# Kernel optimization log

Hardware: AMD Instinct MI355X
Metric: run time of the kernel (lower is better)

The kernel has to match this reference:

```python
import jax, jax.numpy as jnp
import numpy as np

IN_DIM = 2048
OUT_DIM = 2048
BASIS_DIM = 64
BATCH = 4
SEQ = 4096
EPS = 1e-5


def _make_bbasis():
    k = np.arange(BASIS_DIM, dtype=np.float64)[:, None]  # (K,1)
    i = np.arange(OUT_DIM, dtype=np.float64)[None, :]    # (1,D)
    return jnp.asarray(np.cos(2.0 * np.pi * (k + 1.0) / (i + 2.0)), dtype=jnp.float32)


def setup_inputs() -> dict:
    key = jax.random.key(0)
    k1, k2, k3, k4 = jax.random.split(key, 4)
    x = jax.random.normal(k1, (BATCH, SEQ, IN_DIM), dtype=jnp.float32)
    # nn.init.uniform_(-0.1, 0.1) style scaling for weights
    W = jax.random.uniform(k2, (OUT_DIM, IN_DIM), dtype=jnp.float32, minval=-0.1, maxval=0.1)
    W_res = jax.random.uniform(k3, (OUT_DIM, IN_DIM), dtype=jnp.float32, minval=-0.1, maxval=0.1)
    Acoeff = jax.random.uniform(k4, (OUT_DIM, BASIS_DIM), dtype=jnp.float32, minval=-0.1, maxval=0.1)
    gamma = jnp.ones((OUT_DIM,), dtype=jnp.float32)
    beta = jnp.zeros((OUT_DIM,), dtype=jnp.float32)
    Bbasis = _make_bbasis()
    return {"x": x, "W": W, "W_res": W_res, "gamma": gamma, "beta": beta,
            "Acoeff": Acoeff, "Bbasis": Bbasis}


def reference(x, W, W_res, gamma, beta, Acoeff, Bbasis):
    # residual projection (use_residual == 'separate')
    residual = jnp.einsum('bsi,oi->bso', x, W_res)          # (B,S,D)
    transformed = jnp.einsum('bsi,oi->bso', x, W)           # (B,S,D)
    # LayerNorm over last dim
    mean = jnp.mean(transformed, axis=-1, keepdims=True)
    var = jnp.mean(jnp.square(transformed - mean), axis=-1, keepdims=True)
    normalized = (transformed - mean) * jax.lax.rsqrt(var + EPS) * gamma + beta
    # periodic basis gather
    seq_len = x.shape[1]
    j = jnp.arange(seq_len) % BASIS_DIM                      # (S,)
    B_vec = Bbasis[j]                                        # (S,D)
    A_vec = Acoeff[:, j].T                                   # (S,D)
    scalars = jnp.einsum('bsd,sd->bs', normalized, B_vec)    # (B,S)
    return scalars[:, :, None] * A_vec[None] + residual      # (B,S,D)
```

## Files before the change

### kernel.cpp

```cpp
#include <hip/hip_runtime.h>
#include <hip/hip_bf16.h>

#define KDIM   2048
#define DDIM   2048
#define MROWS  16384
#define BASIS  64
#define EPSLN  1e-5f
#define NKT    32

typedef __bf16 bf16x8 __attribute__((ext_vector_type(8)));
typedef float  f32x4  __attribute__((ext_vector_type(4)));
typedef unsigned short u16x8 __attribute__((ext_vector_type(8)));

static __device__ __forceinline__ unsigned short f2bf(float f) {
  union { float f; unsigned int u; } v; v.f = f;
  unsigned int r = v.u + 0x7FFFu + ((v.u >> 16) & 1u);
  return (unsigned short)(r >> 16);
}
static __device__ __forceinline__ float bf2f(unsigned short h) {
  union { unsigned int u; float f; } v; v.u = ((unsigned int)h) << 16;
  return v.f;
}

__global__ __launch_bounds__(256) void cast_f32_bf16(
    const float* __restrict__ in, unsigned short* __restrict__ out, int n4) {
  int i = blockIdx.x * blockDim.x + threadIdx.x;
  int stride = gridDim.x * blockDim.x;
  for (; i < n4; i += stride) {
    float4 v = ((const float4*)in)[i];
    ushort4 o;
    o.x = f2bf(v.x); o.y = f2bf(v.y); o.z = f2bf(v.z); o.w = f2bf(v.w);
    ((ushort4*)out)[i] = o;
  }
}

__global__ __launch_bounds__(256) void transpose_acoeff(
    const float* __restrict__ Ac, float* __restrict__ At) {
  int j = blockIdx.x;
  for (int d = threadIdx.x; d < DDIM; d += blockDim.x)
    At[j * DDIM + d] = Ac[d * BASIS + j];
}

__device__ __forceinline__ void gload16(const void* g, void* l) {
  __builtin_amdgcn_global_load_lds(
      (const __attribute__((address_space(1))) unsigned int*)(unsigned long long)g,
      (__attribute__((address_space(3))) unsigned int*)(unsigned int)(unsigned long long)l,
      16, 0, 0);
}

__device__ __forceinline__ void bar() {
  asm volatile("s_barrier" ::: "memory");
}

__global__ __launch_bounds__(512, 2) void gemm_dual(
    const unsigned short* __restrict__ Abf,
    const unsigned short* __restrict__ Bbf,
    unsigned short* __restrict__ Tout,
    float* __restrict__ Rout)
{
  __shared__ __align__(16) unsigned short As[2 * 256 * 64];
  __shared__ __align__(16) unsigned short Bs[2 * 256 * 64];

  const int tid  = threadIdx.x;
  const int lane = tid & 63;
  const int wave = tid >> 6;

  const int bid = blockIdx.x;
  const int wg  = (bid & 7) * 128 + (bid >> 3);
  const int bm  = wg >> 4;
  const int bn  = wg & 15;
  const int brow0 = bm * 256;
  const int bcol0 = bn * 256;

  const int srow  = tid >> 3;
  const int sslot = (tid & 7) ^ (srow & 7);
  const unsigned short* pA = Abf + (size_t)(brow0 + srow) * KDIM + sslot * 8;
  const unsigned short* pB = Bbf + (size_t)(bcol0 + srow) * KDIM + sslot * 8;
  const int ldst = wave * 512;

  const int wm   = wave >> 2;
  const int wn   = wave & 3;
  const int frow = lane & 15;
  const int kgrp = lane >> 4;
  const int swz  = frow & 7;

  f32x4 acc[8][4] = {};

#pragma unroll
  for (int c = 0; c < 4; ++c) {
    gload16(pA + (size_t)c * 64 * KDIM,      As + c * 4096 + ldst);
    gload16(pB + (size_t)c * 64 * KDIM,      Bs + c * 4096 + ldst);
  }
#pragma unroll
  for (int c = 0; c < 4; ++c) {
    gload16(pA + (size_t)c * 64 * KDIM + 64, As + 16384 + c * 4096 + ldst);
    gload16(pB + (size_t)c * 64 * KDIM + 64, Bs + 16384 + c * 4096 + ldst);
  }

  for (int kt = 0; kt < NKT; ++kt) {
    const unsigned short* As_b = As + (kt & 1) * 16384;
    const unsigned short* Bs_b = Bs + (kt & 1) * 16384;

    if (kt < NKT - 1) { asm volatile("s_waitcnt vmcnt(8)" ::: "memory"); }
    else              { asm volatile("s_waitcnt vmcnt(0)" ::: "memory"); }
    __builtin_amdgcn_sched_barrier(0);
    bar();

#pragma unroll
    for (int ko = 0; ko < 2; ++ko) {
      bf16x8 bv[4], af[4];
#pragma unroll
      for (int j = 0; j < 4; ++j) {
        const int row = wn * 64 + j * 16 + frow;
        bv[j] = *(const bf16x8*)(Bs_b + row * 64 + (((ko * 4 + kgrp) ^ swz) << 3));
      }
#pragma unroll
      for (int i = 0; i < 4; ++i) {
        const int row = wm * 128 + i * 16 + frow;
        af[i] = *(const bf16x8*)(As_b + row * 64 + (((ko * 4 + kgrp) ^ swz) << 3));
      }
      bar();
      __builtin_amdgcn_s_setprio(1);
#pragma unroll
      for (int i = 0; i < 4; ++i)
#pragma unroll
        for (int j = 0; j < 4; ++j)
          acc[i][j] = __builtin_amdgcn_mfma_f32_16x16x32_bf16(af[i], bv[j], acc[i][j], 0, 0, 0);
      __builtin_amdgcn_s_setprio(0);
      bar();
#pragma unroll
      for (int i = 0; i < 4; ++i) {
        const int row = wm * 128 + 64 + i * 16 + frow;
        af[i] = *(const bf16x8*)(As_b + row * 64 + (((ko * 4 + kgrp) ^ swz) << 3));
      }
      bar();
      __builtin_amdgcn_s_setprio(1);
#pragma unroll
      for (int i = 0; i < 4; ++i)
#pragma unroll
        for (int j = 0; j < 4; ++j)
          acc[4 + i][j] = __builtin_amdgcn_mfma_f32_16x16x32_bf16(af[i], bv[j], acc[4 + i][j], 0, 0, 0);
      __builtin_amdgcn_s_setprio(0);
      bar();
    }

    if (kt + 2 < NKT) {
      unsigned short* Ad = As + (kt & 1) * 16384;
      unsigned short* Bd = Bs + (kt & 1) * 16384;
      const int k64 = (kt + 2) * 64;
#pragma unroll
      for (int c = 0; c < 4; ++c) {
        gload16(pA + (size_t)c * 64 * KDIM + k64, Ad + c * 4096 + ldst);
        gload16(pB + (size_t)c * 64 * KDIM + k64, Bd + c * 4096 + ldst);
      }
    }
  }

  if (bn < 8) {
    unsigned short* Cb = Tout;
    const int c0 = bcol0;
#pragma unroll
    for (int i = 0; i < 8; ++i) {
      const int r0 = brow0 + wm * 128 + i * 16 + kgrp * 4;
#pragma unroll
      for (int j = 0; j < 4; ++j) {
        const int col = c0 + wn * 64 + j * 16 + frow;
#pragma unroll
        for (int r = 0; r < 4; ++r)
          Cb[(size_t)(r0 + r) * DDIM + col] = f2bf(acc[i][j][r]);
      }
    }
  } else {
    float* Cb = Rout;
    const int c0 = bcol0 - 2048;
#pragma unroll
    for (int i = 0; i < 8; ++i) {
      const int r0 = brow0 + wm * 128 + i * 16 + kgrp * 4;
#pragma unroll
      for (int j = 0; j < 4; ++j) {
        const int col = c0 + wn * 64 + j * 16 + frow;
#pragma unroll
        for (int r = 0; r < 4; ++r)
          Cb[(size_t)(r0 + r) * DDIM + col] = acc[i][j][r];
      }
    }
  }
}

__global__ __launch_bounds__(256) void epilogue(
    const unsigned short* __restrict__ T, const float* __restrict__ Bb,
    const float* __restrict__ At, const float* __restrict__ gam,
    const float* __restrict__ bet, float* __restrict__ out)
{
  __shared__ float red[16];
  const int row = blockIdx.x;
  const int s   = row & 4095;
  const int j   = s & 63;
  const int tid = threadIdx.x;
  const size_t rb = (size_t)row * DDIM;
  const int d0 = tid * 8;

  u16x8 tv = *(const u16x8*)(T + rb + d0);
  float t[8];
#pragma unroll
  for (int k = 0; k < 8; ++k) t[k] = bf2f(tv[k]);

  float sum = 0.f, sq = 0.f;
#pragma unroll
  for (int k = 0; k < 8; ++k) { sum += t[k]; sq += t[k] * t[k]; }
#pragma unroll
  for (int off = 32; off > 0; off >>= 1) {
    sum += __shfl_down(sum, off);
    sq  += __shfl_down(sq,  off);
  }
  if ((tid & 63) == 0) { red[tid >> 6] = sum; red[4 + (tid >> 6)] = sq; }
  __syncthreads();
  if (tid == 0) {
    float sAll = red[0] + red[1] + red[2] + red[3];
    float qAll = red[4] + red[5] + red[6] + red[7];
    float m = sAll * (1.0f / 2048.0f);
    float v = qAll * (1.0f / 2048.0f) - m * m;
    red[8] = m;
    red[9] = rsqrtf(v + EPSLN);
  }
  __syncthreads();
  const float mean = red[8], rstd = red[9];

  const size_t jb = (size_t)j * DDIM;
  float4 g0 = *(const float4*)(gam + d0), g1 = *(const float4*)(gam + d0 + 4);
  float4 b0 = *(const float4*)(bet + d0), b1 = *(const float4*)(bet + d0 + 4);
  float4 w0 = *(const float4*)(Bb + jb + d0), w1 = *(const float4*)(Bb + jb + d0 + 4);

  float sc =
      ((t[0] - mean) * rstd * g0.x + b0.x) * w0.x +
      ((t[1] - mean) * rstd * g0.y + b0.y) * w0.y +
      ((t[2] - mean) * rstd * g0.z + b0.z) * w0.z +
      ((t[3] - mean) * rstd * g0.w + b0.w) * w0.w +
      ((t[4] - mean) * rstd * g1.x + b1.x) * w1.x +
      ((t[5] - mean) * rstd * g1.y + b1.y) * w1.y +
      ((t[6] - mean) * rstd * g1.z + b1.z) * w1.z +
      ((t[7] - mean) * rstd * g1.w + b1.w) * w1.w;
#pragma unroll
  for (int off = 32; off > 0; off >>= 1) sc += __shfl_down(sc, off);
  if ((tid & 63) == 0) red[10 + (tid >> 6)] = sc;
  __syncthreads();
  const float scalar = red[10] + red[11] + red[12] + red[13];

  float4 a0 = *(const float4*)(At + jb + d0), a1 = *(const float4*)(At + jb + d0 + 4);
  float4 o0 = *(const float4*)(out + rb + d0), o1 = *(const float4*)(out + rb + d0 + 4);
  o0.x = scalar * a0.x + o0.x;  o0.y = scalar * a0.y + o0.y;
  o0.z = scalar * a0.z + o0.z;  o0.w = scalar * a0.w + o0.w;
  o1.x = scalar * a1.x + o1.x;  o1.y = scalar * a1.y + o1.y;
  o1.z = scalar * a1.z + o1.z;  o1.w = scalar * a1.w + o1.w;
  *(float4*)(out + rb + d0)     = o0;
  *(float4*)(out + rb + d0 + 4) = o1;
}

extern "C" void kernel_launch(void* const* d_in, const int* in_sizes, int n_in,
                              void* d_out, int out_size, void* d_ws, size_t ws_size,
                              hipStream_t stream) {
  const float* x      = (const float*)d_in[0];
  const float* W      = (const float*)d_in[1];
  const float* Wres   = (const float*)d_in[2];
  const float* gamma  = (const float*)d_in[3];
  const float* beta   = (const float*)d_in[4];
  const float* Acoeff = (const float*)d_in[5];
  const float* Bbasis = (const float*)d_in[6];
  float* out = (float*)d_out;
  char* ws = (char*)d_ws;

  unsigned short* xbf = (unsigned short*)ws;
  unsigned short* Wc  = (unsigned short*)(ws + 67108864);
  unsigned short* T   = (unsigned short*)(ws + 83886080);
  float* At           = (float*)(ws + 150994944);

  cast_f32_bf16<<<2048, 256, 0, stream>>>(x,    xbf,            8388608);
  cast_f32_bf16<<<512,  256, 0, stream>>>(W,    Wc,             1048576);
  cast_f32_bf16<<<512,  256, 0, stream>>>(Wres, Wc + 4194304,   1048576);
  transpose_acoeff<<<64, 256, 0, stream>>>(Acoeff, At);

  gemm_dual<<<1024, 512, 0, stream>>>(xbf, Wc, T, out);

  epilogue<<<16384, 256, 0, stream>>>(T, Bbasis, At, gamma, beta, out);
}
```

Baseline: 612.2 us.

## Fuse prep kernels, interleave GEMM prefetch with MFMA phases, store residual as bf16

Merges the three cast launches and the Acoeff transpose into one prep kernel. Restructures the GEMM main loop into four MFMA phases, spreading the next-tile global-to-LDS loads across them instead of issuing them all at the end of each k-step. The residual half of the GEMM output is now written as bf16 to a workspace buffer, and the epilogue reads it back instead of round-tripping fp32 through the output. This cuts the residual's write and read traffic in half but adds bf16 rounding to the residual term.

```diff
diff --git a/kernel.cpp b/kernel.cpp
--- a/kernel.cpp
+++ b/kernel.cpp
@@ -22,23 +22,38 @@
   return v.f;
 }
 
-__global__ __launch_bounds__(256) void cast_f32_bf16(
-    const float* __restrict__ in, unsigned short* __restrict__ out, int n4) {
-  int i = blockIdx.x * blockDim.x + threadIdx.x;
-  int stride = gridDim.x * blockDim.x;
-  for (; i < n4; i += stride) {
-    float4 v = ((const float4*)in)[i];
-    ushort4 o;
-    o.x = f2bf(v.x); o.y = f2bf(v.y); o.z = f2bf(v.z); o.w = f2bf(v.w);
-    ((ushort4*)out)[i] = o;
-  }
-}
-
-__global__ __launch_bounds__(256) void transpose_acoeff(
-    const float* __restrict__ Ac, float* __restrict__ At) {
-  int j = blockIdx.x;
-  for (int d = threadIdx.x; d < DDIM; d += blockDim.x)
-    At[j * DDIM + d] = Ac[d * BASIS + j];
+__global__ __launch_bounds__(256) void prep(
+    const float* __restrict__ x, const float* __restrict__ W,
+    const float* __restrict__ Wres, const float* __restrict__ Ac,
+    unsigned short* __restrict__ xbf, unsigned short* __restrict__ Wc,
+    float* __restrict__ At) {
+  const int b = blockIdx.x, t = threadIdx.x;
+  if (b < 2048) {
+    const float4* in = (const float4*)x;
+    ushort4* op = (ushort4*)xbf;
+    const int base = b * 4096;
+#pragma unroll
+    for (int k = 0; k < 16; ++k) {
+      const int i = base + k * 256 + t;
+      float4 v = in[i];
+      op[i] = make_ushort4(f2bf(v.x), f2bf(v.y), f2bf(v.z), f2bf(v.w));
+    }
+  } else if (b < 3072) {
+    const bool isW = (b < 2560);
+    const float4* in = (const float4*)(isW ? W : Wres);
+    ushort4* op = (ushort4*)(Wc + (isW ? 0 : 4194304));
+    const int base = (isW ? (b - 2048) : (b - 2560)) * 2048;
+#pragma unroll
+    for (int k = 0; k < 8; ++k) {
+      const int i = base + k * 256 + t;
+      float4 v = in[i];
+      op[i] = make_ushort4(f2bf(v.x), f2bf(v.y), f2bf(v.z), f2bf(v.w));
+    }
+  } else {
+    const int j = b - 3072;
+    for (int d = t; d < DDIM; d += 256)
+      At[j * DDIM + d] = Ac[d * BASIS + j];
+  }
 }
 
 __device__ __forceinline__ void gload16(const void* g, void* l) {
@@ -47,16 +62,13 @@
       (__attribute__((address_space(3))) unsigned int*)(unsigned int)(unsigned long long)l,
       16, 0, 0);
 }
-
-__device__ __forceinline__ void bar() {
-  asm volatile("s_barrier" ::: "memory");
-}
+__device__ __forceinline__ void bar() { asm volatile("s_barrier" ::: "memory"); }
 
 __global__ __launch_bounds__(512, 2) void gemm_dual(
     const unsigned short* __restrict__ Abf,
     const unsigned short* __restrict__ Bbf,
     unsigned short* __restrict__ Tout,
-    float* __restrict__ Rout)
+    unsigned short* __restrict__ Rout)
 {
   __shared__ __align__(16) unsigned short As[2 * 256 * 64];
   __shared__ __align__(16) unsigned short Bs[2 * 256 * 64];
@@ -82,115 +94,123 @@
   const int wn   = wave & 3;
   const int frow = lane & 15;
   const int kgrp = lane >> 4;
-  const int swz  = frow & 7;
+
+#define SA(d, kk, c) gload16(pA + (size_t)(c)*64*KDIM + (kk)*64, As + (d)*16384 + (c)*4096 + ldst)
+#define SB(d, kk, c) gload16(pB + (size_t)(c)*64*KDIM + (kk)*64, Bs + (d)*16384 + (c)*4096 + ldst)
+#define RD_A(mf, kc) (*(const bf16x8*)(Ard + (wm*128 + (mf)*16 + frow)*64 + ((((kc)*4 + kgrp) ^ (frow & 7)) << 3)))
+#define RD_B(j, kc)  (*(const bf16x8*)(Brd + (wn*64  + (j)*16  + frow)*64 + ((((kc)*4 + kgrp) ^ (frow & 7)) << 3)))
 
   f32x4 acc[8][4] = {};
 
-#pragma unroll
-  for (int c = 0; c < 4; ++c) {
-    gload16(pA + (size_t)c * 64 * KDIM,      As + c * 4096 + ldst);
-    gload16(pB + (size_t)c * 64 * KDIM,      Bs + c * 4096 + ldst);
-  }
-#pragma unroll
-  for (int c = 0; c < 4; ++c) {
-    gload16(pA + (size_t)c * 64 * KDIM + 64, As + 16384 + c * 4096 + ldst);
-    gload16(pB + (size_t)c * 64 * KDIM + 64, Bs + 16384 + c * 4096 + ldst);
-  }
+  SA(0,0,0); SA(0,0,1); SA(0,0,2); SA(0,0,3);
+  SB(0,0,0); SB(0,0,1); SB(0,0,2); SB(0,0,3);
+  SB(1,1,0); SB(1,1,1);
+  SA(1,1,0); SA(1,1,2);
+  SB(1,1,2); SB(1,1,3);
+  asm volatile("s_waitcnt vmcnt(6)" ::: "memory");
+  __builtin_amdgcn_sched_barrier(0);
+  bar();
 
   for (int kt = 0; kt < NKT; ++kt) {
-    const unsigned short* As_b = As + (kt & 1) * 16384;
-    const unsigned short* Bs_b = Bs + (kt & 1) * 16384;
-
-    if (kt < NKT - 1) { asm volatile("s_waitcnt vmcnt(8)" ::: "memory"); }
+    const int d = kt & 1;
+    const unsigned short* Ard = As + d * 16384;
+    const unsigned short* Brd = Bs + d * 16384;
+
+    bf16x8 bv[4][2], af0[2], af1[2];
+
+#pragma unroll
+    for (int j = 0; j < 4; ++j) { bv[j][0] = RD_B(j, 0); bv[j][1] = RD_B(j, 1); }
+    af0[0] = RD_A(0, 0); af0[1] = RD_A(0, 1);
+    af1[0] = RD_A(1, 0); af1[1] = RD_A(1, 1);
+    if (kt < NKT - 1) { SA(d ^ 1, kt + 1, 1); SA(d ^ 1, kt + 1, 3); }
+    bar();
+    __builtin_amdgcn_s_setprio(1);
+#pragma unroll
+    for (int j = 0; j < 4; ++j) {
+      acc[0][j] = __builtin_amdgcn_mfma_f32_16x16x32_bf16(af0[0], bv[j][0], acc[0][j], 0, 0, 0);
+      acc[0][j] = __builtin_amdgcn_mfma_f32_16x16x32_bf16(af0[1], bv[j][1], acc[0][j], 0, 0, 0);
+      acc[1][j] = __builtin_amdgcn_mfma_f32_16x16x32_bf16(af1[0], bv[j][0], acc[1][j], 0, 0, 0);
+      acc[1][j] = __builtin_amdgcn_mfma_f32_16x16x32_bf16(af1[1], bv[j][1], acc[1][j], 0, 0, 0);
+    }
+    __builtin_amdgcn_s_setprio(0);
+    __builtin_amdgcn_sched_barrier(0);
+    bar();
+
+    af0[0] = RD_A(2, 0); af0[1] = RD_A(2, 1);
+    af1[0] = RD_A(3, 0); af1[1] = RD_A(3, 1);
+    if (kt < NKT - 2) { SB(d, kt + 2, 0); SB(d, kt + 2, 1); }
+    bar();
+    __builtin_amdgcn_s_setprio(1);
+#pragma unroll
+    for (int j = 0; j < 4; ++j) {
+      acc[2][j] = __builtin_amdgcn_mfma_f32_16x16x32_bf16(af0[0], bv[j][0], acc[2][j], 0, 0, 0);
+      acc[2][j] = __builtin_amdgcn_mfma_f32_16x16x32_bf16(af0[1], bv[j][1], acc[2][j], 0, 0, 0);
+      acc[3][j] = __builtin_amdgcn_mfma_f32_16x16x32_bf16(af1[0], bv[j][0], acc[3][j], 0, 0, 0);
+      acc[3][j] = __builtin_amdgcn_mfma_f32_16x16x32_bf16(af1[1], bv[j][1], acc[3][j], 0, 0, 0);
+    }
+    __builtin_amdgcn_s_setprio(0);
+    __builtin_amdgcn_sched_barrier(0);
+    bar();
+
+    af0[0] = RD_A(4, 0); af0[1] = RD_A(4, 1);
+    af1[0] = RD_A(5, 0); af1[1] = RD_A(5, 1);
+    if (kt < NKT - 2) { SA(d, kt + 2, 0); SA(d, kt + 2, 2); }
+    bar();
+    __builtin_amdgcn_s_setprio(1);
+#pragma unroll
+    for (int j = 0; j < 4; ++j) {
+      acc[4][j] = __builtin_amdgcn_mfma_f32_16x16x32_bf16(af0[0], bv[j][0], acc[4][j], 0, 0, 0);
+      acc[4][j] = __builtin_amdgcn_mfma_f32_16x16x32_bf16(af0[1], bv[j][1], acc[4][j], 0, 0, 0);
+      acc[5][j] = __builtin_amdgcn_mfma_f32_16x16x32_bf16(af1[0], bv[j][0], acc[5][j], 0, 0, 0);
+      acc[5][j] = __builtin_amdgcn_mfma_f32_16x16x32_bf16(af1[1], bv[j][1], acc[5][j], 0, 0, 0);
+    }
+    __builtin_amdgcn_s_setprio(0);
+    __builtin_amdgcn_sched_barrier(0);
+    bar();
+
+    af0[0] = RD_A(6, 0); af0[1] = RD_A(6, 1);
+    af1[0] = RD_A(7, 0); af1[1] = RD_A(7, 1);
+    if (kt < NKT - 2) { SB(d, kt + 2, 2); SB(d, kt + 2, 3); }
+    bar();
+    __builtin_amdgcn_s_setprio(1);
+#pragma unroll
+    for (int j = 0; j < 4; ++j) {
+      acc[6][j] = __builtin_amdgcn_mfma_f32_16x16x32_bf16(af0[0], bv[j][0], acc[6][j], 0, 0, 0);
+      acc[6][j] = __builtin_amdgcn_mfma_f32_16x16x32_bf16(af0[1], bv[j][1], acc[6][j], 0, 0, 0);
+      acc[7][j] = __builtin_amdgcn_mfma_f32_16x16x32_bf16(af1[0], bv[j][0], acc[7][j], 0, 0, 0);
+      acc[7][j] = __builtin_amdgcn_mfma_f32_16x16x32_bf16(af1[1], bv[j][1], acc[7][j], 0, 0, 0);
+    }
+    __builtin_amdgcn_s_setprio(0);
+    if (kt < NKT - 2) { asm volatile("s_waitcnt vmcnt(6)" ::: "memory"); }
     else              { asm volatile("s_waitcnt vmcnt(0)" ::: "memory"); }
     __builtin_amdgcn_sched_barrier(0);
     bar();
-
-#pragma unroll
-    for (int ko = 0; ko < 2; ++ko) {
-      bf16x8 bv[4], af[4];
-#pragma unroll
-      for (int j = 0; j < 4; ++j) {
-        const int row = wn * 64 + j * 16 + frow;
-        bv[j] = *(const bf16x8*)(Bs_b + row * 64 + (((ko * 4 + kgrp) ^ swz) << 3));
-      }
-#pragma unroll
-      for (int i = 0; i < 4; ++i) {
-        const int row = wm * 128 + i * 16 + frow;
-        af[i] = *(const bf16x8*)(As_b + row * 64 + (((ko * 4 + kgrp) ^ swz) << 3));
-      }
-      bar();
-      __builtin_amdgcn_s_setprio(1);
-#pragma unroll
-      for (int i = 0; i < 4; ++i)
-#pragma unroll
-        for (int j = 0; j < 4; ++j)
-          acc[i][j] = __builtin_amdgcn_mfma_f32_16x16x32_bf16(af[i], bv[j], acc[i][j], 0, 0, 0);
-      __builtin_amdgcn_s_setprio(0);
-      bar();
-#pragma unroll
-      for (int i = 0; i < 4; ++i) {
-        const int row = wm * 128 + 64 + i * 16 + frow;
-        af[i] = *(const bf16x8*)(As_b + row * 64 + (((ko * 4 + kgrp) ^ swz) << 3));
-      }
-      bar();
-      __builtin_amdgcn_s_setprio(1);
-#pragma unroll
-      for (int i = 0; i < 4; ++i)
-#pragma unroll
-        for (int j = 0; j < 4; ++j)
-          acc[4 + i][j] = __builtin_amdgcn_mfma_f32_16x16x32_bf16(af[i], bv[j], acc[4 + i][j], 0, 0, 0);
-      __builtin_amdgcn_s_setprio(0);
-      bar();
-    }
-
-    if (kt + 2 < NKT) {
-      unsigned short* Ad = As + (kt & 1) * 16384;
-      unsigned short* Bd = Bs + (kt & 1) * 16384;
-      const int k64 = (kt + 2) * 64;
-#pragma unroll
-      for (int c = 0; c < 4; ++c) {
-        gload16(pA + (size_t)c * 64 * KDIM + k64, Ad + c * 4096 + ldst);
-        gload16(pB + (size_t)c * 64 * KDIM + k64, Bd + c * 4096 + ldst);
-      }
-    }
-  }
-
-  if (bn < 8) {
-    unsigned short* Cb = Tout;
-    const int c0 = bcol0;
-#pragma unroll
-    for (int i = 0; i < 8; ++i) {
-      const int r0 = brow0 + wm * 128 + i * 16 + kgrp * 4;
-#pragma unroll
-      for (int j = 0; j < 4; ++j) {
-        const int col = c0 + wn * 64 + j * 16 + frow;
-#pragma unroll
-        for (int r = 0; r < 4; ++r)
-          Cb[(size_t)(r0 + r) * DDIM + col] = f2bf(acc[i][j][r]);
-      }
-    }
-  } else {
-    float* Cb = Rout;
-    const int c0 = bcol0 - 2048;
-#pragma unroll
-    for (int i = 0; i < 8; ++i) {
-      const int r0 = brow0 + wm * 128 + i * 16 + kgrp * 4;
-#pragma unroll
-      for (int j = 0; j < 4; ++j) {
-        const int col = c0 + wn * 64 + j * 16 + frow;
-#pragma unroll
-        for (int r = 0; r < 4; ++r)
-          Cb[(size_t)(r0 + r) * DDIM + col] = acc[i][j][r];
-      }
-    }
-  }
+  }
+
+  unsigned short* Cb = (bn < 8) ? Tout : Rout;
+  const int c0 = (bn < 8) ? bcol0 : (bcol0 - 2048);
+#pragma unroll
+  for (int i = 0; i < 8; ++i) {
+    const int r0 = brow0 + wm * 128 + i * 16 + kgrp * 4;
+#pragma unroll
+    for (int j = 0; j < 4; ++j) {
+      const int col = c0 + wn * 64 + j * 16 + frow;
+#pragma unroll
+      for (int r = 0; r < 4; ++r)
+        Cb[(size_t)(r0 + r) * DDIM + col] = f2bf(acc[i][j][r]);
+    }
+  }
+#undef SA
+#undef SB
+#undef RD_A
+#undef RD_B
 }
 
 __global__ __launch_bounds__(256) void epilogue(
-    const unsigned short* __restrict__ T, const float* __restrict__ Bb,
-    const float* __restrict__ At, const float* __restrict__ gam,
-    const float* __restrict__ bet, float* __restrict__ out)
+    const unsigned short* __restrict__ T, const unsigned short* __restrict__ R,
+    const float* __restrict__ Bb, const float* __restrict__ At,
+    const float* __restrict__ gam, const float* __restrict__ bet,
+    float* __restrict__ out)
 {
   __shared__ float red[16];
   const int row = blockIdx.x;
@@ -246,12 +266,13 @@
   __syncthreads();
   const float scalar = red[10] + red[11] + red[12] + red[13];
 
+  u16x8 rv = *(const u16x8*)(R + rb + d0);
   float4 a0 = *(const float4*)(At + jb + d0), a1 = *(const float4*)(At + jb + d0 + 4);
-  float4 o0 = *(const float4*)(out + rb + d0), o1 = *(const float4*)(out + rb + d0 + 4);
-  o0.x = scalar * a0.x + o0.x;  o0.y = scalar * a0.y + o0.y;
-  o0.z = scalar * a0.z + o0.z;  o0.w = scalar * a0.w + o0.w;
-  o1.x = scalar * a1.x + o1.x;  o1.y = scalar * a1.y + o1.y;
-  o1.z = scalar * a1.z + o1.z;  o1.w = scalar * a1.w + o1.w;
+  float4 o0, o1;
+  o0.x = scalar * a0.x + bf2f(rv[0]);  o0.y = scalar * a0.y + bf2f(rv[1]);
+  o0.z = scalar * a0.z + bf2f(rv[2]);  o0.w = scalar * a0.w + bf2f(rv[3]);
+  o1.x = scalar * a1.x + bf2f(rv[4]);  o1.y = scalar * a1.y + bf2f(rv[5]);
+  o1.z = scalar * a1.z + bf2f(rv[6]);  o1.w = scalar * a1.w + bf2f(rv[7]);
   *(float4*)(out + rb + d0)     = o0;
   *(float4*)(out + rb + d0 + 4) = o1;
 }
@@ -272,14 +293,12 @@
   unsigned short* xbf = (unsigned short*)ws;
   unsigned short* Wc  = (unsigned short*)(ws + 67108864);
   unsigned short* T   = (unsigned short*)(ws + 83886080);
-  float* At           = (float*)(ws + 150994944);
-
-  cast_f32_bf16<<<2048, 256, 0, stream>>>(x,    xbf,            8388608);
-  cast_f32_bf16<<<512,  256, 0, stream>>>(W,    Wc,             1048576);
-  cast_f32_bf16<<<512,  256, 0, stream>>>(Wres, Wc + 4194304,   1048576);
-  transpose_acoeff<<<64, 256, 0, stream>>>(Acoeff, At);
-
-  gemm_dual<<<1024, 512, 0, stream>>>(xbf, Wc, T, out);
-
-  epilogue<<<16384, 256, 0, stream>>>(T, Bbasis, At, gamma, beta, out);
-}
+  unsigned short* Rbf = (unsigned short*)(ws + 150994944);
+  float* At           = (float*)(ws + 218103808);
+
+  prep<<<3136, 256, 0, stream>>>(x, W, Wres, Acoeff, xbf, Wc, At);
+
+  gemm_dual<<<1024, 512, 0, stream>>>(xbf, Wc, T, Rbf);
+
+  epilogue<<<16384, 256, 0, stream>>>(T, Rbf, Bbasis, At, gamma, beta, out);
+}
```

Result: faster. 538.9 us (-12.0%).
